# Kernel tuning notes

Hardware: AMD Instinct MI355X
Metric: run time of the kernel (lower is better)

Reference implementation:

```python
import jax, jax.numpy as jnp
import numpy as np
import math

N = 100000      # num vertices
M = 50000       # num hyperedges
NNZ = 800000    # incidence entries
F_IN = 128
NHID = 128
NCLS = 40
DEPTH = 4
ALPHA = 0.1     # restart_alpha
LAMDA = 0.5


def setup_inputs() -> dict:
    key = jax.random.key(0)
    ks = jax.random.split(key, 8)
    x = jax.random.normal(ks[0], (N, F_IN), jnp.float32)
    vertex = jax.random.randint(ks[1], (NNZ,), 0, N)
    edges = jax.random.randint(ks[2], (NNZ,), 0, M)
    s0 = 1.0 / np.sqrt(F_IN)
    sh = 1.0 / np.sqrt(NHID)
    W0 = jax.random.uniform(ks[3], (F_IN, NHID), jnp.float32, -s0, s0)
    b0 = jax.random.uniform(ks[4], (NHID,), jnp.float32, -s0, s0)
    Ws = jax.random.uniform(ks[5], (DEPTH, NHID, NHID), jnp.float32, -sh, sh)
    Wout = jax.random.uniform(ks[6], (NHID, NCLS), jnp.float32, -sh, sh)
    bout = jax.random.uniform(ks[7], (NCLS,), jnp.float32, -sh, sh)
    return {"x": x, "W0": W0, "b0": b0, "Ws": Ws, "Wout": Wout,
            "bout": bout, "vertex": vertex, "edges": edges}


def reference(x, W0, b0, Ws, Wout, bout, vertex, edges):
    ones = jnp.ones((NNZ, 1), x.dtype)
    cnt_e = jnp.maximum(jax.ops.segment_sum(ones, edges, num_segments=M), 1.0)
    cnt_v = jnp.maximum(jax.ops.segment_sum(ones, vertex, num_segments=N), 1.0)

    x = jax.nn.relu(x @ W0 + b0)
    x0 = x
    for i in range(DEPTH):
        beta = math.log(LAMDA / (i + 1) + 1.0)
        # vertex -> edge mean aggregation
        Xve = x[vertex]                                          # [NNZ, NHID]
        Xe = jax.ops.segment_sum(Xve, edges, num_segments=M) / cnt_e
        # edge -> vertex mean aggregation
        Xev = Xe[edges]                                          # [NNZ, NHID]
        Xv = jax.ops.segment_sum(Xev, vertex, num_segments=N) / cnt_v
        # L2 row-normalize with detached scale (use_norm=True)
        norm = jnp.linalg.norm(Xv, axis=1, keepdims=True)
        scale = jax.lax.stop_gradient(jnp.where(norm > 0, 1.0 / norm, 0.0))
        Xv = Xv * scale
        # alpha/beta residual blend (UniGCNII)
        Xi = (1.0 - ALPHA) * Xv + ALPHA * x0
        x = jax.nn.relu((1.0 - beta) * Xi + beta * (Xi @ Ws[i]))
    return x @ Wout + bout
```

## Files before the change

### kernel.cpp

```cpp
#include <hip/hip_runtime.h>

#define NV 100000
#define NE 50000
#define NNZ_C 800000
#define CAP_E 64
#define CAP_V 48
#define NB_E 391
#define NB_V 782
#define CAPB_E8 512
#define CAPB_V8 256
#define OVF_CAP 810000
#define NCUR ((NB_E + NB_V) * 8)
#define OVCNT_E NCUR
#define OVCNT_V (NCUR + 1)

typedef unsigned int uint32;
typedef unsigned short u16;
typedef u16 u16x8 __attribute__((ext_vector_type(8)));
typedef short short8 __attribute__((ext_vector_type(8)));
typedef float floatx16 __attribute__((ext_vector_type(16)));

__device__ __forceinline__ float bf2f(u16 h) {
  return __uint_as_float(((uint32)h) << 16);
}
__device__ __forceinline__ u16 f2bf(float f) {
  uint32 u = __float_as_uint(f);
  u += 0x7FFF + ((u >> 16) & 1);
  return (u16)(u >> 16);
}
__device__ __forceinline__ int xcc_id() {
  int x;
  asm("s_getreg_b32 %0, hwreg(HW_REG_XCC_ID)" : "=s"(x));
  return x & 7;
}


__global__ void zero_misc(int* __restrict__ bcur, int nb,
                          u16* __restrict__ dummyX, u16* __restrict__ dummyXe) {
  int i = blockIdx.x * blockDim.x + threadIdx.x;
  if (i < nb) bcur[i] = 0;
  if (i < 128) { dummyX[i] = 0; dummyXe[i] = 0; }
}


__global__ void bucket_scatter(const int* __restrict__ vertex, const int* __restrict__ edges,
                               int* __restrict__ bcur,
                               uint32* __restrict__ pairE, uint32* __restrict__ pairV,
                               uint2* __restrict__ ovfE, uint2* __restrict__ ovfV) {
  int xcd = xcc_id();
  int stride = gridDim.x * blockDim.x;
  const int half = NNZ_C / 2;
  for (int k = blockIdx.x * blockDim.x + threadIdx.x; k < half; k += stride) {
    uint32 e0 = (uint32)edges[k],        v0 = (uint32)vertex[k];
    uint32 e1 = (uint32)edges[k + half], v1 = (uint32)vertex[k + half];
    uint32 be0 = e0 >> 7, bv0 = v0 >> 7, be1 = e1 >> 7, bv1 = v1 >> 7;
    int se0 = (int)(be0 * 8) + xcd, sv0 = (int)(bv0 * 8) + xcd;
    int se1 = (int)(be1 * 8) + xcd, sv1 = (int)(bv1 * 8) + xcd;
    int pe0 = atomicAdd(&bcur[se0 << 4], 1);
    int pv0 = atomicAdd(&bcur[(NB_E * 8 + sv0) << 4], 1);
    int pe1 = atomicAdd(&bcur[se1 << 4], 1);
    int pv1 = atomicAdd(&bcur[(NB_E * 8 + sv1) << 4], 1);
    uint32 pkE0 = ((e0 & 127u) << 25) | v0, pkV0 = ((v0 & 127u) << 25) | e0;
    uint32 pkE1 = ((e1 & 127u) << 25) | v1, pkV1 = ((v1 & 127u) << 25) | e1;
    if (pe0 < CAPB_E8) pairE[(size_t)se0 * CAPB_E8 + pe0] = pkE0;
    else { int op = atomicAdd(&bcur[OVCNT_E << 4], 1); if (op < OVF_CAP) ovfE[op] = make_uint2(be0, pkE0); }
    if (pv0 < CAPB_V8) pairV[(size_t)sv0 * CAPB_V8 + pv0] = pkV0;
    else { int op = atomicAdd(&bcur[OVCNT_V << 4], 1); if (op < OVF_CAP) ovfV[op] = make_uint2(bv0, pkV0); }
    if (pe1 < CAPB_E8) pairE[(size_t)se1 * CAPB_E8 + pe1] = pkE1;
    else { int op = atomicAdd(&bcur[OVCNT_E << 4], 1); if (op < OVF_CAP) ovfE[op] = make_uint2(be1, pkE1); }
    if (pv1 < CAPB_V8) pairV[(size_t)sv1 * CAPB_V8 + pv1] = pkV1;
    else { int op = atomicAdd(&bcur[OVCNT_V << 4], 1); if (op < OVF_CAP) ovfV[op] = make_uint2(bv1, pkV1); }
  }
}

__global__ __launch_bounds__(256) void expand(const uint32* __restrict__ pairs,
                                              const int* __restrict__ bcur, int subOff,
                                              int capb, const uint2* __restrict__ ovf,
                                              int ovfIdx, int* __restrict__ items, int cap,
                                              int* __restrict__ cnt, int nKeys,
                                              int P, int dummy) {
  __shared__ int lcnt[128];
  int b = blockIdx.x, t = threadIdx.x;
  if (t < 128) lcnt[t] = 0;
  __syncthreads();
  #pragma unroll
  for (int x = 0; x < 8; x++) {
    int c = subOff + b * 8 + x;
    int n = min(bcur[c << 4], capb);
    const uint32* p = pairs + (size_t)(b * 8 + x) * capb;
    for (int i = t; i < n; i += 256) {
      uint32 w = p[i];
      int loc = w >> 25;
      int val = (int)(w & 0x1FFFFFFu);
      int r = atomicAdd(&lcnt[loc], 1);
      if (r < cap) items[(size_t)((b << 7) + loc) * cap + r] = val;
    }
  }
  int novf = min(bcur[ovfIdx << 4], OVF_CAP);
  for (int i = t; i < novf; i += 256) {
    uint2 w = ovf[i];
    if ((int)w.x == b) {
      int loc = w.y >> 25;
      int val = (int)(w.y & 0x1FFFFFFu);
      int r = atomicAdd(&lcnt[loc], 1);
      if (r < cap) items[(size_t)((b << 7) + loc) * cap + r] = val;
    }
  }
  __syncthreads();
  if (t < 128) {
    int key = (b << 7) + t;
    if (key < nKeys) {
      int c = lcnt[t];
      cnt[key] = c;
      int cc = min(c, cap);
      int padded = min((cc + P - 1) & ~(P - 1), cap);
      for (int r = cc; r < padded; r++)
        items[(size_t)key * cap + r] = dummy;
    }
  }
}


__global__ void prep_weights(const float* __restrict__ W0, const float* __restrict__ Ws,
                             u16* __restrict__ WT) {
  int idx = blockIdx.x * blockDim.x + threadIdx.x;
  if (idx >= 5 * 16384) return;
  const float betas[4] = {0.4054651081f, 0.2231435513f, 0.1541506798f, 0.1177830357f};
  int sec = idx >> 14;
  int rc = idx & 16383;
  int n = rc >> 7, k = rc & 127;
  float v;
  if (sec == 0) {
    v = W0[k * 128 + n];
  } else {
    int i = sec - 1;
    float b = betas[i];
    v = b * Ws[i * 16384 + k * 128 + n];
    if (k == n) v += 1.0f - b;
  }
  WT[idx] = f2bf(v);
}


__global__ __launch_bounds__(256) void edge_agg(const u16* __restrict__ Xh,
                                                const int* __restrict__ cntE,
                                                const int* __restrict__ itemsE,
                                                u16* __restrict__ Xeh) {
  int g = threadIdx.x >> 4;
  int lane = threadIdx.x & 15;
  int e = blockIdx.x * 16 + g;
  int cnt = cntE[e];
  int n16 = (min(cnt, CAP_E) + 15) & ~15;
  const int* it = itemsE + (size_t)e * CAP_E;
  float acc[8] = {0.f, 0.f, 0.f, 0.f, 0.f, 0.f, 0.f, 0.f};
  for (int j = 0; j < n16; j += 16) {
    int4 i0 = *(const int4*)(it + j);
    int4 i1 = *(const int4*)(it + j + 4);
    int4 i2 = *(const int4*)(it + j + 8);
    int4 i3 = *(const int4*)(it + j + 12);
    u16x8 r0 = *(const u16x8*)(Xh + (size_t)i0.x * 128 + lane * 8);
    u16x8 r1 = *(const u16x8*)(Xh + (size_t)i0.y * 128 + lane * 8);
    u16x8 r2 = *(const u16x8*)(Xh + (size_t)i0.z * 128 + lane * 8);
    u16x8 r3 = *(const u16x8*)(Xh + (size_t)i0.w * 128 + lane * 8);
    u16x8 r4 = *(const u16x8*)(Xh + (size_t)i1.x * 128 + lane * 8);
    u16x8 r5 = *(const u16x8*)(Xh + (size_t)i1.y * 128 + lane * 8);
    u16x8 r6 = *(const u16x8*)(Xh + (size_t)i1.z * 128 + lane * 8);
    u16x8 r7 = *(const u16x8*)(Xh + (size_t)i1.w * 128 + lane * 8);
    u16x8 r8 = *(const u16x8*)(Xh + (size_t)i2.x * 128 + lane * 8);
    u16x8 r9 = *(const u16x8*)(Xh + (size_t)i2.y * 128 + lane * 8);
    u16x8 rA = *(const u16x8*)(Xh + (size_t)i2.z * 128 + lane * 8);
    u16x8 rB = *(const u16x8*)(Xh + (size_t)i2.w * 128 + lane * 8);
    u16x8 rC = *(const u16x8*)(Xh + (size_t)i3.x * 128 + lane * 8);
    u16x8 rD = *(const u16x8*)(Xh + (size_t)i3.y * 128 + lane * 8);
    u16x8 rE = *(const u16x8*)(Xh + (size_t)i3.z * 128 + lane * 8);
    u16x8 rF = *(const u16x8*)(Xh + (size_t)i3.w * 128 + lane * 8);
    #pragma unroll
    for (int q = 0; q < 8; q++) {
      float s0 = (bf2f(r0[q]) + bf2f(r1[q])) + (bf2f(r2[q]) + bf2f(r3[q]));
      float s1 = (bf2f(r4[q]) + bf2f(r5[q])) + (bf2f(r6[q]) + bf2f(r7[q]));
      float s2 = (bf2f(r8[q]) + bf2f(r9[q])) + (bf2f(rA[q]) + bf2f(rB[q]));
      float s3 = (bf2f(rC[q]) + bf2f(rD[q])) + (bf2f(rE[q]) + bf2f(rF[q]));
      acc[q] += (s0 + s1) + (s2 + s3);
    }
  }
  float inv = 1.f / fmaxf((float)cnt, 1.f);
  u16x8 o;
  #pragma unroll
  for (int q = 0; q < 8; q++) o[q] = f2bf(acc[q] * inv);
  *(u16x8*)(Xeh + (size_t)e * 128 + lane * 8) = o;
}

__global__ __launch_bounds__(256) void vertex_agg(const u16* __restrict__ Xeh,
                                                  const int* __restrict__ cntV,
                                                  const int* __restrict__ itemsV,
                                                  const u16* __restrict__ x0h,
                                                  u16* __restrict__ Xih) {
  int g = threadIdx.x >> 4;
  int lane = threadIdx.x & 15;
  int v = blockIdx.x * 16 + g;
  int cnt = cntV[v];
  int n8 = (min(cnt, CAP_V) + 7) & ~7;
  const int* it = itemsV + (size_t)v * CAP_V;
  float acc[8] = {0.f, 0.f, 0.f, 0.f, 0.f, 0.f, 0.f, 0.f};
  for (int j = 0; j < n8; j += 8) {
    int4 e0 = *(const int4*)(it + j);
    int4 e1 = *(const int4*)(it + j + 4);
    u16x8 r0 = *(const u16x8*)(Xeh + (size_t)e0.x * 128 + lane * 8);
    u16x8 r1 = *(const u16x8*)(Xeh + (size_t)e0.y * 128 + lane * 8);
    u16x8 r2 = *(const u16x8*)(Xeh + (size_t)e0.z * 128 + lane * 8);
    u16x8 r3 = *(const u16x8*)(Xeh + (size_t)e0.w * 128 + lane * 8);
    u16x8 r4 = *(const u16x8*)(Xeh + (size_t)e1.x * 128 + lane * 8);
    u16x8 r5 = *(const u16x8*)(Xeh + (size_t)e1.y * 128 + lane * 8);
    u16x8 r6 = *(const u16x8*)(Xeh + (size_t)e1.z * 128 + lane * 8);
    u16x8 r7 = *(const u16x8*)(Xeh + (size_t)e1.w * 128 + lane * 8);
    #pragma unroll
    for (int q = 0; q < 8; q++)
      acc[q] += ((bf2f(r0[q]) + bf2f(r1[q])) + (bf2f(r2[q]) + bf2f(r3[q]))) +
                ((bf2f(r4[q]) + bf2f(r5[q])) + (bf2f(r6[q]) + bf2f(r7[q])));
  }
  float inv = 1.f / fmaxf((float)cnt, 1.f);
  float sq = 0.f;
  #pragma unroll
  for (int q = 0; q < 8; q++) { acc[q] *= inv; sq += acc[q] * acc[q]; }
  sq += __shfl_xor(sq, 1, 64);
  sq += __shfl_xor(sq, 2, 64);
  sq += __shfl_xor(sq, 4, 64);
  sq += __shfl_xor(sq, 8, 64);
  float scale = (sq > 0.f) ? rsqrtf(sq) : 0.f;
  u16x8 x0v = *(const u16x8*)(x0h + (size_t)v * 128 + lane * 8);
  u16x8 o;
  #pragma unroll
  for (int q = 0; q < 8; q++)
    o[q] = f2bf(0.9f * acc[q] * scale + 0.1f * bf2f(x0v[q]));
  *(u16x8*)(Xih + (size_t)v * 128 + lane * 8) = o;
}


__global__ __launch_bounds__(256) void gemm_mfma(const u16* __restrict__ Ah,
                                                 const u16* __restrict__ WT,
                                                 u16* __restrict__ Yh, int nrows) {
  __shared__ u16 As[128 * 136];
  __shared__ u16 Bs[128 * 136];
  int t = threadIdx.x;
  int row0 = blockIdx.x * 128;
  #pragma unroll
  for (int i = 0; i < 8; i++) {
    int idx = t + 256 * i;
    int r = idx >> 4, c8 = idx & 15;
    u16x8 v = {0, 0, 0, 0, 0, 0, 0, 0};
    if (row0 + r < nrows) v = *(const u16x8*)(Ah + (size_t)(row0 + r) * 128 + c8 * 8);
    *(u16x8*)&As[r * 136 + c8 * 8] = v;
    *(u16x8*)&Bs[r * 136 + c8 * 8] = *(const u16x8*)(WT + (size_t)r * 128 + c8 * 8);
  }
  __syncthreads();

  int w = t >> 6, lane = t & 63;
  int l31 = lane & 31, kh = lane >> 5;
  int wr = w >> 1, wc = w & 1;
  floatx16 acc[2][2];
  #pragma unroll
  for (int rt = 0; rt < 2; rt++)
    #pragma unroll
    for (int ct = 0; ct < 2; ct++)
      #pragma unroll
      for (int q = 0; q < 16; q++) acc[rt][ct][q] = 0.f;

  #pragma unroll
  for (int ks = 0; ks < 8; ks++) {
    int koff = ks * 16 + kh * 8;
    short8 a0 = *(const short8*)&As[(wr * 64 + l31) * 136 + koff];
    short8 a1 = *(const short8*)&As[(wr * 64 + 32 + l31) * 136 + koff];
    short8 b0 = *(const short8*)&Bs[(wc * 64 + l31) * 136 + koff];
    short8 b1 = *(const short8*)&Bs[(wc * 64 + 32 + l31) * 136 + koff];
    acc[0][0] = __builtin_amdgcn_mfma_f32_32x32x16_bf16(a0, b0, acc[0][0], 0, 0, 0);
    acc[0][1] = __builtin_amdgcn_mfma_f32_32x32x16_bf16(a0, b1, acc[0][1], 0, 0, 0);
    acc[1][0] = __builtin_amdgcn_mfma_f32_32x32x16_bf16(a1, b0, acc[1][0], 0, 0, 0);
    acc[1][1] = __builtin_amdgcn_mfma_f32_32x32x16_bf16(a1, b1, acc[1][1], 0, 0, 0);
  }
  __syncthreads();

  #pragma unroll
  for (int rt = 0; rt < 2; rt++)
    #pragma unroll
    for (int ct = 0; ct < 2; ct++) {
      int col = wc * 64 + ct * 32 + l31;
      #pragma unroll
      for (int reg = 0; reg < 16; reg++) {
        int row = wr * 64 + rt * 32 + (reg & 3) + 8 * (reg >> 2) + 4 * kh;
        As[row * 136 + col] = f2bf(fmaxf(acc[rt][ct][reg], 0.f));
      }
    }
  __syncthreads();
  #pragma unroll
  for (int i = 0; i < 8; i++) {
    int idx = t + 256 * i;
    int r = idx >> 4, c8 = idx & 15;
    if (row0 + r < nrows)
      *(u16x8*)(Yh + (size_t)(row0 + r) * 128 + c8 * 8) =
          *(const u16x8*)&As[r * 136 + c8 * 8];
  }
}

__global__ __launch_bounds__(256) void gemm_first(const float* __restrict__ A,
                                                  const u16* __restrict__ WT,
                                                  const float* __restrict__ bias,
                                                  u16* __restrict__ Yh,
                                                  u16* __restrict__ Y2h, int nrows) {
  __shared__ u16 As[128 * 136];
  __shared__ u16 Bs[128 * 136];
  int t = threadIdx.x;
  int row0 = blockIdx.x * 128;
  #pragma unroll
  for (int i = 0; i < 8; i++) {
    int idx = t + 256 * i;
    int r = idx >> 4, c8 = idx & 15;
    u16x8 v = {0, 0, 0, 0, 0, 0, 0, 0};
    if (row0 + r < nrows) {
      const float* p = A + (size_t)(row0 + r) * 128 + c8 * 8;
      float4 a = *(const float4*)p;
      float4 b = *(const float4*)(p + 4);
      v[0] = f2bf(a.x); v[1] = f2bf(a.y); v[2] = f2bf(a.z); v[3] = f2bf(a.w);
      v[4] = f2bf(b.x); v[5] = f2bf(b.y); v[6] = f2bf(b.z); v[7] = f2bf(b.w);
    }
    *(u16x8*)&As[r * 136 + c8 * 8] = v;
    *(u16x8*)&Bs[r * 136 + c8 * 8] = *(const u16x8*)(WT + (size_t)r * 128 + c8 * 8);
  }
  __syncthreads();

  int w = t >> 6, lane = t & 63;
  int l31 = lane & 31, kh = lane >> 5;
  int wr = w >> 1, wc = w & 1;
  floatx16 acc[2][2];
  #pragma unroll
  for (int rt = 0; rt < 2; rt++)
    #pragma unroll
    for (int ct = 0; ct < 2; ct++)
      #pragma unroll
      for (int q = 0; q < 16; q++) acc[rt][ct][q] = 0.f;

  #pragma unroll
  for (int ks = 0; ks < 8; ks++) {
    int koff = ks * 16 + kh * 8;
    short8 a0 = *(const short8*)&As[(wr * 64 + l31) * 136 + koff];
    short8 a1 = *(const short8*)&As[(wr * 64 + 32 + l31) * 136 + koff];
    short8 b0 = *(const short8*)&Bs[(wc * 64 + l31) * 136 + koff];
    short8 b1 = *(const short8*)&Bs[(wc * 64 + 32 + l31) * 136 + koff];
    acc[0][0] = __builtin_amdgcn_mfma_f32_32x32x16_bf16(a0, b0, acc[0][0], 0, 0, 0);
    acc[0][1] = __builtin_amdgcn_mfma_f32_32x32x16_bf16(a0, b1, acc[0][1], 0, 0, 0);
    acc[1][0] = __builtin_amdgcn_mfma_f32_32x32x16_bf16(a1, b0, acc[1][0], 0, 0, 0);
    acc[1][1] = __builtin_amdgcn_mfma_f32_32x32x16_bf16(a1, b1, acc[1][1], 0, 0, 0);
  }
  __syncthreads();

  #pragma unroll
  for (int rt = 0; rt < 2; rt++)
    #pragma unroll
    for (int ct = 0; ct < 2; ct++) {
      int col = wc * 64 + ct * 32 + l31;
      float bv = bias[col];
      #pragma unroll
      for (int reg = 0; reg < 16; reg++) {
        int row = wr * 64 + rt * 32 + (reg & 3) + 8 * (reg >> 2) + 4 * kh;
        As[row * 136 + col] = f2bf(fmaxf(acc[rt][ct][reg] + bv, 0.f));
      }
    }
  __syncthreads();
  #pragma unroll
  for (int i = 0; i < 8; i++) {
    int idx = t + 256 * i;
    int r = idx >> 4, c8 = idx & 15;
    if (row0 + r < nrows) {
      u16x8 v = *(const u16x8*)&As[r * 136 + c8 * 8];
      *(u16x8*)(Yh + (size_t)(row0 + r) * 128 + c8 * 8) = v;
      *(u16x8*)(Y2h + (size_t)(row0 + r) * 128 + c8 * 8) = v;
    }
  }
}


__global__ __launch_bounds__(256) void gemm_out(const u16* __restrict__ Xh,
                                                const float* __restrict__ W,
                                                const float* __restrict__ bias,
                                                float* __restrict__ Y, int nrows) {
  __shared__ float xs[128][36];
  __shared__ float ws[32][44];
  int t = threadIdx.x;
  int tr = t >> 3;
  int tc = t & 7;
  int row0 = blockIdx.x * 128;
  float acc[4][5];
  #pragma unroll
  for (int i = 0; i < 4; i++)
    #pragma unroll
    for (int j = 0; j < 5; j++) acc[i][j] = 0.f;

  for (int k0 = 0; k0 < 128; k0 += 32) {
    #pragma unroll
    for (int i = 0; i < 2; i++) {
      int idx = t + 256 * i;
      int r = idx >> 2, c8 = idx & 3;
      int gr = row0 + r;
      u16x8 v = {0, 0, 0, 0, 0, 0, 0, 0};
      if (gr < nrows) v = *(const u16x8*)(Xh + (size_t)gr * 128 + k0 + c8 * 8);
      #pragma unroll
      for (int q = 0; q < 8; q++) xs[r][c8 * 8 + q] = bf2f(v[q]);
    }
    #pragma unroll
    for (int i = 0; i < 5; i++) {
      int idx = t + 256 * i;
      int r = idx / 40, c = idx % 40;
      ws[r][c] = W[(k0 + r) * 40 + c];
    }
    __syncthreads();
    #pragma unroll
    for (int kk4 = 0; kk4 < 8; kk4++) {
      float4 xv[4];
      #pragma unroll
      for (int i = 0; i < 4; i++) xv[i] = *(const float4*)&xs[tr + 32 * i][kk4 * 4];
      #pragma unroll
      for (int q = 0; q < 4; q++) {
        int kk = kk4 * 4 + q;
        float wv[5];
        #pragma unroll
        for (int j = 0; j < 5; j++) wv[j] = ws[kk][tc * 5 + j];
        #pragma unroll
        for (int i = 0; i < 4; i++) {
          float xq = ((const float*)&xv[i])[q];
          #pragma unroll
          for (int j = 0; j < 5; j++) acc[i][j] += xq * wv[j];
        }
      }
    }
    __syncthreads();
  }
  #pragma unroll
  for (int i = 0; i < 4; i++) {
    int gr = row0 + tr + 32 * i;
    if (gr >= nrows) continue;
    #pragma unroll
    for (int j = 0; j < 5; j++) {
      int c = tc * 5 + j;
      Y[(long)gr * 40 + c] = acc[i][j] + bias[c];
    }
  }
}


extern "C" void kernel_launch(void* const* d_in, const int* in_sizes, int n_in,
                              void* d_out, int out_size, void* d_ws, size_t ws_size,
                              hipStream_t stream) {
  const float* x    = (const float*)d_in[0];
  const float* W0   = (const float*)d_in[1];
  const float* b0   = (const float*)d_in[2];
  const float* Ws   = (const float*)d_in[3];
  const float* Wout = (const float*)d_in[4];
  const float* bout = (const float*)d_in[5];
  const int* vertex = (const int*)d_in[6];
  const int* edges  = (const int*)d_in[7];
  float* out = (float*)d_out;

  char* base = (char*)d_ws;
  size_t o = 0;
  auto alloc = [&](size_t bytes) -> char* {
    char* r = base + o;
    o += (bytes + 255) & ~(size_t)255;
    return r;
  };
  u16* x_curh = (u16*)alloc((size_t)(NV + 1) * 128 * 2);
  u16* x0h    = (u16*)alloc((size_t)NV * 128 * 2);
  u16* Xeh    = (u16*)alloc((size_t)(NE + 1) * 128 * 2);
  u16* WT     = (u16*)alloc((size_t)5 * 16384 * 2);
  int* cntE   = (int*)alloc((size_t)NE * 4);
  int* cntV   = (int*)alloc((size_t)NV * 4);
  int* itemsE = (int*)alloc((size_t)NE * CAP_E * 4);
  int* itemsV = (int*)alloc((size_t)NV * CAP_V * 4);
  uint32* pairE = (uint32*)alloc((size_t)NB_E * 8 * CAPB_E8 * 4);
  uint32* pairV = (uint32*)alloc((size_t)NB_V * 8 * CAPB_V8 * 4);
  uint2* ovfE  = (uint2*)alloc((size_t)OVF_CAP * 8);
  uint2* ovfV  = (uint2*)alloc((size_t)OVF_CAP * 8);
  int* bcur   = (int*)alloc((size_t)(NCUR + 2) * 16 * 4);

  int nb = (NCUR + 2) * 16;
  zero_misc<<<(nb + 255) / 256, 256, 0, stream>>>(bcur, nb,
                                                  x_curh + (size_t)NV * 128,
                                                  Xeh + (size_t)NE * 128);
  bucket_scatter<<<1024, 256, 0, stream>>>(vertex, edges, bcur, pairE, pairV, ovfE, ovfV);
  expand<<<NB_E, 256, 0, stream>>>(pairE, bcur, 0, CAPB_E8, ovfE, OVCNT_E,
                                   itemsE, CAP_E, cntE, NE, 16, NV);
  expand<<<NB_V, 256, 0, stream>>>(pairV, bcur, NB_E * 8, CAPB_V8, ovfV, OVCNT_V,
                                   itemsV, CAP_V, cntV, NV, 8, NE);
  prep_weights<<<(5 * 16384 + 255) / 256, 256, 0, stream>>>(W0, Ws, WT);

  int gblocks = (NV + 127) / 128;
  gemm_first<<<gblocks, 256, 0, stream>>>(x, WT, b0, x_curh, x0h, NV);

  for (int i = 0; i < 4; i++) {
    edge_agg<<<NE / 16, 256, 0, stream>>>(x_curh, cntE, itemsE, Xeh);
    vertex_agg<<<NV / 16, 256, 0, stream>>>(Xeh, cntV, itemsV, x0h, x_curh);
    gemm_mfma<<<gblocks, 256, 0, stream>>>(x_curh, WT + (size_t)(1 + i) * 16384,
                                           x_curh, NV);
  }
  gemm_out<<<gblocks, 256, 0, stream>>>(x_curh, Wout, bout, out, NV);
}
```

Before: 555.2 us.

## Replace per-XCD global atomic bucket scatter with tile-local histogram binning

The preprocessing scatter now works on 4096-element tiles per block. Each block builds shared-memory histograms of edge and vertex buckets, then reserves space in one global counter per bucket with a single atomic, and writes pairs at the reserved offsets. This replaces the old per-element global atomics on padded per-XCD counters, cutting global atomic traffic. Bucket capacities become per-bucket (2560/1408), and the expand kernel reads one contiguous segment instead of eight sub-buckets.

```diff
diff --git a/kernel.cpp b/kernel.cpp
--- a/kernel.cpp
+++ b/kernel.cpp
@@ -7,12 +7,11 @@
 #define CAP_V 48
 #define NB_E 391
 #define NB_V 782
-#define CAPB_E8 512
-#define CAPB_V8 256
+#define CAPB_E 2560
+#define CAPB_V 1408
 #define OVF_CAP 810000
-#define NCUR ((NB_E + NB_V) * 8)
-#define OVCNT_E NCUR
-#define OVCNT_V (NCUR + 1)
+#define T_ITEMS 4096
+#define N_TILES ((NNZ_C + T_ITEMS - 1) / T_ITEMS)
 
 typedef unsigned int uint32;
 typedef unsigned short u16;
@@ -28,75 +27,94 @@
   u += 0x7FFF + ((u >> 16) & 1);
   return (u16)(u >> 16);
 }
-__device__ __forceinline__ int xcc_id() {
-  int x;
-  asm("s_getreg_b32 %0, hwreg(HW_REG_XCC_ID)" : "=s"(x));
-  return x & 7;
-}
-
-
-__global__ void zero_misc(int* __restrict__ bcur, int nb,
+
+
+__global__ void zero_misc(int* __restrict__ cur, int n,
                           u16* __restrict__ dummyX, u16* __restrict__ dummyXe) {
   int i = blockIdx.x * blockDim.x + threadIdx.x;
-  if (i < nb) bcur[i] = 0;
+  if (i < n) cur[i] = 0;
   if (i < 128) { dummyX[i] = 0; dummyXe[i] = 0; }
 }
 
 
-__global__ void bucket_scatter(const int* __restrict__ vertex, const int* __restrict__ edges,
-                               int* __restrict__ bcur,
-                               uint32* __restrict__ pairE, uint32* __restrict__ pairV,
-                               uint2* __restrict__ ovfE, uint2* __restrict__ ovfV) {
-  int xcd = xcc_id();
-  int stride = gridDim.x * blockDim.x;
-  const int half = NNZ_C / 2;
-  for (int k = blockIdx.x * blockDim.x + threadIdx.x; k < half; k += stride) {
-    uint32 e0 = (uint32)edges[k],        v0 = (uint32)vertex[k];
-    uint32 e1 = (uint32)edges[k + half], v1 = (uint32)vertex[k + half];
-    uint32 be0 = e0 >> 7, bv0 = v0 >> 7, be1 = e1 >> 7, bv1 = v1 >> 7;
-    int se0 = (int)(be0 * 8) + xcd, sv0 = (int)(bv0 * 8) + xcd;
-    int se1 = (int)(be1 * 8) + xcd, sv1 = (int)(bv1 * 8) + xcd;
-    int pe0 = atomicAdd(&bcur[se0 << 4], 1);
-    int pv0 = atomicAdd(&bcur[(NB_E * 8 + sv0) << 4], 1);
-    int pe1 = atomicAdd(&bcur[se1 << 4], 1);
-    int pv1 = atomicAdd(&bcur[(NB_E * 8 + sv1) << 4], 1);
-    uint32 pkE0 = ((e0 & 127u) << 25) | v0, pkV0 = ((v0 & 127u) << 25) | e0;
-    uint32 pkE1 = ((e1 & 127u) << 25) | v1, pkV1 = ((v1 & 127u) << 25) | e1;
-    if (pe0 < CAPB_E8) pairE[(size_t)se0 * CAPB_E8 + pe0] = pkE0;
-    else { int op = atomicAdd(&bcur[OVCNT_E << 4], 1); if (op < OVF_CAP) ovfE[op] = make_uint2(be0, pkE0); }
-    if (pv0 < CAPB_V8) pairV[(size_t)sv0 * CAPB_V8 + pv0] = pkV0;
-    else { int op = atomicAdd(&bcur[OVCNT_V << 4], 1); if (op < OVF_CAP) ovfV[op] = make_uint2(bv0, pkV0); }
-    if (pe1 < CAPB_E8) pairE[(size_t)se1 * CAPB_E8 + pe1] = pkE1;
-    else { int op = atomicAdd(&bcur[OVCNT_E << 4], 1); if (op < OVF_CAP) ovfE[op] = make_uint2(be1, pkE1); }
-    if (pv1 < CAPB_V8) pairV[(size_t)sv1 * CAPB_V8 + pv1] = pkV1;
-    else { int op = atomicAdd(&bcur[OVCNT_V << 4], 1); if (op < OVF_CAP) ovfV[op] = make_uint2(bv1, pkV1); }
+__global__ __launch_bounds__(256) void scatter_binned(const int* __restrict__ vertex,
+                                                      const int* __restrict__ edges,
+                                                      int* __restrict__ curE,
+                                                      int* __restrict__ curV,
+                                                      int* __restrict__ ovfCnt,
+                                                      uint32* __restrict__ pairE,
+                                                      uint32* __restrict__ pairV,
+                                                      uint2* __restrict__ ovfE,
+                                                      uint2* __restrict__ ovfV) {
+  __shared__ int histE[NB_E], baseE[NB_E];
+  __shared__ int histV[NB_V], baseV[NB_V];
+  int t = threadIdx.x;
+  for (int tile = blockIdx.x; tile < N_TILES; tile += gridDim.x) {
+    for (int b = t; b < NB_E; b += 256) histE[b] = 0;
+    for (int b = t; b < NB_V; b += 256) histV[b] = 0;
+    __syncthreads();
+    int base = tile * T_ITEMS;
+    int ev[16], vv[16], rE[16], rV[16];
+    #pragma unroll
+    for (int i = 0; i < 16; i++) {
+      int k = base + t + i * 256;
+      if (k < NNZ_C) {
+        ev[i] = edges[k];
+        vv[i] = vertex[k];
+        rE[i] = atomicAdd(&histE[ev[i] >> 7], 1);
+        rV[i] = atomicAdd(&histV[vv[i] >> 7], 1);
+      }
+    }
+    __syncthreads();
+    for (int b = t; b < NB_E; b += 256) {
+      int h = histE[b];
+      baseE[b] = h ? atomicAdd(&curE[b], h) : 0;
+    }
+    for (int b = t; b < NB_V; b += 256) {
+      int h = histV[b];
+      baseV[b] = h ? atomicAdd(&curV[b], h) : 0;
+    }
+    __syncthreads();
+    #pragma unroll
+    for (int i = 0; i < 16; i++) {
+      int k = base + t + i * 256;
+      if (k < NNZ_C) {
+        uint32 e = (uint32)ev[i], v = (uint32)vv[i];
+        uint32 pkE = ((e & 127u) << 25) | v;
+        uint32 pkV = ((v & 127u) << 25) | e;
+        int pE = baseE[e >> 7] + rE[i];
+        if (pE < CAPB_E) pairE[(size_t)(e >> 7) * CAPB_E + pE] = pkE;
+        else { int op = atomicAdd(&ovfCnt[0], 1); if (op < OVF_CAP) ovfE[op] = make_uint2(e >> 7, pkE); }
+        int pV = baseV[v >> 7] + rV[i];
+        if (pV < CAPB_V) pairV[(size_t)(v >> 7) * CAPB_V + pV] = pkV;
+        else { int op = atomicAdd(&ovfCnt[1], 1); if (op < OVF_CAP) ovfV[op] = make_uint2(v >> 7, pkV); }
+      }
+    }
+    __syncthreads();
   }
 }
 
 __global__ __launch_bounds__(256) void expand(const uint32* __restrict__ pairs,
-                                              const int* __restrict__ bcur, int subOff,
-                                              int capb, const uint2* __restrict__ ovf,
-                                              int ovfIdx, int* __restrict__ items, int cap,
+                                              const int* __restrict__ cur, int capb,
+                                              const uint2* __restrict__ ovf,
+                                              const int* __restrict__ ovfCnt,
+                                              int* __restrict__ items, int cap,
                                               int* __restrict__ cnt, int nKeys,
                                               int P, int dummy) {
   __shared__ int lcnt[128];
   int b = blockIdx.x, t = threadIdx.x;
   if (t < 128) lcnt[t] = 0;
   __syncthreads();
-  #pragma unroll
-  for (int x = 0; x < 8; x++) {
-    int c = subOff + b * 8 + x;
-    int n = min(bcur[c << 4], capb);
-    const uint32* p = pairs + (size_t)(b * 8 + x) * capb;
-    for (int i = t; i < n; i += 256) {
-      uint32 w = p[i];
-      int loc = w >> 25;
-      int val = (int)(w & 0x1FFFFFFu);
-      int r = atomicAdd(&lcnt[loc], 1);
-      if (r < cap) items[(size_t)((b << 7) + loc) * cap + r] = val;
-    }
-  }
-  int novf = min(bcur[ovfIdx << 4], OVF_CAP);
+  int n = min(cur[b], capb);
+  const uint32* p = pairs + (size_t)b * capb;
+  for (int i = t; i < n; i += 256) {
+    uint32 w = p[i];
+    int loc = w >> 25;
+    int val = (int)(w & 0x1FFFFFFu);
+    int r = atomicAdd(&lcnt[loc], 1);
+    if (r < cap) items[(size_t)((b << 7) + loc) * cap + r] = val;
+  }
+  int novf = min(*ovfCnt, OVF_CAP);
   for (int i = t; i < novf; i += 256) {
     uint2 w = ovf[i];
     if ((int)w.x == b) {
@@ -474,20 +492,24 @@
   int* cntV   = (int*)alloc((size_t)NV * 4);
   int* itemsE = (int*)alloc((size_t)NE * CAP_E * 4);
   int* itemsV = (int*)alloc((size_t)NV * CAP_V * 4);
-  uint32* pairE = (uint32*)alloc((size_t)NB_E * 8 * CAPB_E8 * 4);
-  uint32* pairV = (uint32*)alloc((size_t)NB_V * 8 * CAPB_V8 * 4);
+  uint32* pairE = (uint32*)alloc((size_t)NB_E * CAPB_E * 4);
+  uint32* pairV = (uint32*)alloc((size_t)NB_V * CAPB_V * 4);
   uint2* ovfE  = (uint2*)alloc((size_t)OVF_CAP * 8);
   uint2* ovfV  = (uint2*)alloc((size_t)OVF_CAP * 8);
-  int* bcur   = (int*)alloc((size_t)(NCUR + 2) * 16 * 4);
-
-  int nb = (NCUR + 2) * 16;
-  zero_misc<<<(nb + 255) / 256, 256, 0, stream>>>(bcur, nb,
-                                                  x_curh + (size_t)NV * 128,
-                                                  Xeh + (size_t)NE * 128);
-  bucket_scatter<<<1024, 256, 0, stream>>>(vertex, edges, bcur, pairE, pairV, ovfE, ovfV);
-  expand<<<NB_E, 256, 0, stream>>>(pairE, bcur, 0, CAPB_E8, ovfE, OVCNT_E,
+  int* curAll = (int*)alloc((size_t)(NB_E + NB_V + 2) * 4);
+  int* curE = curAll;
+  int* curV = curAll + NB_E;
+  int* ovfCnt = curAll + NB_E + NB_V;
+
+  int nzero = NB_E + NB_V + 2;
+  zero_misc<<<(nzero + 255) / 256, 256, 0, stream>>>(curAll, nzero,
+                                                     x_curh + (size_t)NV * 128,
+                                                     Xeh + (size_t)NE * 128);
+  scatter_binned<<<N_TILES, 256, 0, stream>>>(vertex, edges, curE, curV, ovfCnt,
+                                              pairE, pairV, ovfE, ovfV);
+  expand<<<NB_E, 256, 0, stream>>>(pairE, curE, CAPB_E, ovfE, ovfCnt,
                                    itemsE, CAP_E, cntE, NE, 16, NV);
-  expand<<<NB_V, 256, 0, stream>>>(pairV, bcur, NB_E * 8, CAPB_V8, ovfV, OVCNT_V,
+  expand<<<NB_V, 256, 0, stream>>>(pairV, curV, CAPB_V, ovfV, ovfCnt + 1,
                                    itemsV, CAP_V, cntV, NV, 8, NE);
   prep_weights<<<(5 * 16384 + 255) / 256, 256, 0, stream>>>(W0, Ws, WT);
 
```

New measurement: 503.4 us. 9.3% less time.
